# Kernel tuning notes

Hardware: AMD Instinct MI355X
Metric: run time of the kernel (lower is better)

The kernel has to match this reference:

```python
import jax, jax.numpy as jnp
import numpy as np

B, S, D = 8, 1024, 1024      # batch, seq, input_dim (= d_model)
H, E = 16, 64                # n_heads, d_embed (H*E == D)


def setup_inputs() -> dict:
    key = jax.random.key(0)
    ks = jax.random.split(key, 12)
    sd = 1.0 / np.sqrt(D)
    inp = {
        "X1": jax.random.normal(ks[0], (B, S, D), jnp.float32),
        "X2": jax.random.normal(ks[1], (B, S, D), jnp.float32),
        # Linear params stored as [in, out]
        "Wq": jax.random.uniform(ks[2], (D, H * E), jnp.float32, -sd, sd),
        "bq": jax.random.uniform(ks[3], (H * E,), jnp.float32, -sd, sd),
        "Wk": jax.random.uniform(ks[4], (D, H * E), jnp.float32, -sd, sd),
        "bk": jax.random.uniform(ks[5], (H * E,), jnp.float32, -sd, sd),
        "Wv": jax.random.uniform(ks[6], (D, H * E), jnp.float32, -sd, sd),
        "bv": jax.random.uniform(ks[7], (H * E,), jnp.float32, -sd, sd),
        "Wo": jax.random.uniform(ks[8], (H * E, D), jnp.float32, -sd, sd),
        "bo": jax.random.uniform(ks[9], (D,), jnp.float32, -sd, sd),
    }
    return inp


def reference(X1, X2, Wq, bq, Wk, bk, Wv, bv, Wo, bo):
    b, s, _ = X1.shape

    def split(x):  # [B,S,H*E] -> [B,H,S,E]
        return x.reshape(b, s, H, E).transpose(0, 2, 1, 3)

    Q = split(X1 @ Wq + bq)
    K = split(X2 @ Wk + bk)
    V = split(X2 @ Wv + bv)

    # Faithful quirk: d_k = K.shape[0] AFTER split_heads == batch size
    scores = jnp.einsum("bhqe,bhke->bhqk", Q, K) / jnp.sqrt(jnp.float32(b))

    # masked=True: tril then replace exact zeros with -1e9 (source quirk)
    tri = jnp.tril(jnp.ones((s, s), jnp.float32))
    scores = scores * tri
    scores = jnp.where(scores == 0.0, jnp.float32(-1e9), scores)

    # torch.nn.Softmax() with no dim on 4D input -> legacy dim=1 (heads axis)
    attn = jax.nn.softmax(scores, axis=1)

    out = jnp.einsum("bhqk,bhke->bhqe", attn, V)
    out = out.transpose(0, 2, 1, 3).reshape(b, s, H * E)  # combine heads
    return out @ Wo + bo
```

## Files before the change

kernel.cpp:

```cpp
#include <hip/hip_runtime.h>
#include <cstdint>


typedef unsigned short u16;
typedef unsigned int   u32;
typedef __attribute__((ext_vector_type(8))) __bf16         bf16x8;
typedef __attribute__((ext_vector_type(8))) unsigned short ushort8;
typedef __attribute__((ext_vector_type(4))) float          f32x4;

#define S_ 1024
#define D_ 1024
#define H_ 16
#define E_ 64

__device__ __forceinline__ float b2f(u16 h) {
  union { u32 u; float f; } v; v.u = ((u32)h) << 16; return v.f;
}
__device__ __forceinline__ u16 f2b(float f) {
  union { float f; u32 u; } v; v.f = f;
  u32 r = v.u + 0x7fffu + ((v.u >> 16) & 1u);
  return (u16)(r >> 16);
}

typedef const __attribute__((address_space(1))) u32 gu32;
typedef       __attribute__((address_space(3))) u32 lu32;

__device__ __forceinline__ void gload_lds16(const u16* g, u16* l) {
  __builtin_amdgcn_global_load_lds((gu32*)(uintptr_t)g, (lu32*)(uintptr_t)l,
                                   16, 0, 0);
}

__global__ __launch_bounds__(256, 1) void cvt_bf16(
    const float* __restrict__ src, u16* __restrict__ dst)
{
  const size_t i = (size_t)blockIdx.x * 256 + threadIdx.x;
  float4 a = ((const float4*)src)[2 * i];
  float4 b = ((const float4*)src)[2 * i + 1];
  ushort8 o;
  o[0] = f2b(a.x); o[1] = f2b(a.y); o[2] = f2b(a.z); o[3] = f2b(a.w);
  o[4] = f2b(b.x); o[5] = f2b(b.y); o[6] = f2b(b.z); o[7] = f2b(b.w);
  ((ushort8*)dst)[i] = o;
}

__global__ __launch_bounds__(256, 1) void trans_cvt_w(
    const float* __restrict__ W, u16* __restrict__ Wt)
{
  __shared__ u16 t[64][72];
  const int k0 = blockIdx.x * 64, n0 = blockIdx.y * 64;
  const int row = threadIdx.x >> 3;
  const int cs  = (threadIdx.x & 7) * 8;
#pragma unroll
  for (int p = 0; p < 2; ++p) {
    int r = row + p * 32;
    const float* Wp = W + (size_t)(k0 + r) * 1024 + n0 + cs;
    float4 a = *(const float4*)(Wp);
    float4 b = *(const float4*)(Wp + 4);
    u16* tp = &t[r][cs];
    tp[0] = f2b(a.x); tp[1] = f2b(a.y); tp[2] = f2b(a.z); tp[3] = f2b(a.w);
    tp[4] = f2b(b.x); tp[5] = f2b(b.y); tp[6] = f2b(b.z); tp[7] = f2b(b.w);
  }
  __syncthreads();
#pragma unroll
  for (int p = 0; p < 2; ++p) {
    int n = row + p * 32;
    ushort8 v;
#pragma unroll
    for (int i = 0; i < 8; ++i) v[i] = t[cs + i][n];
    *(ushort8*)(Wt + (size_t)(n0 + n) * 1024 + k0 + cs) = v;
  }
}

__global__ __launch_bounds__(256, 1) void gemm_bf16(
    const u16* __restrict__ A, const u16* __restrict__ Bt,
    const float* __restrict__ bias, void* __restrict__ Cv,
    int M, int N, int K, int out_f32)
{
  __shared__ u16 As[128 * 32];
  __shared__ u16 Bs[128 * 32];
  const int tid  = threadIdx.x;
  const int wave = tid >> 6;
  const int lane = tid & 63;
  const int quad = lane >> 4;
  const int l16  = lane & 15;
  const int m0   = (wave & 1) * 64;
  const int n0   = (wave >> 1) * 64;

  const u16* Ab = A  + (size_t)blockIdx.x * 128 * K;
  const u16* Bb = Bt + (size_t)blockIdx.y * 128 * K;

  f32x4 acc[4][4];
#pragma unroll
  for (int i = 0; i < 4; ++i)
#pragma unroll
    for (int j = 0; j < 4; ++j) acc[i][j] = (f32x4){0.f, 0.f, 0.f, 0.f};

  for (int kb = 0; kb < K; kb += 32) {
    __syncthreads();
#pragma unroll
    for (int p = 0; p < 2; ++p) {
      int seg = tid + p * 256;
      int row = seg >> 2, ks = seg & 3;
      gload_lds16(Ab + (size_t)row * K + kb + ks * 8, As + seg * 8);
      gload_lds16(Bb + (size_t)row * K + kb + ks * 8, Bs + seg * 8);
    }
    __builtin_amdgcn_s_waitcnt(0);
    __syncthreads();

    bf16x8 af[4], bfr[4];
#pragma unroll
    for (int i = 0; i < 4; ++i)
      af[i] = *(const bf16x8*)(As + (m0 + i * 16 + l16) * 32 + quad * 8);
#pragma unroll
    for (int j = 0; j < 4; ++j)
      bfr[j] = *(const bf16x8*)(Bs + (n0 + j * 16 + l16) * 32 + quad * 8);
#pragma unroll
    for (int i = 0; i < 4; ++i)
#pragma unroll
      for (int j = 0; j < 4; ++j)
        acc[i][j] = __builtin_amdgcn_mfma_f32_16x16x32_bf16(
            af[i], bfr[j], acc[i][j], 0, 0, 0);
  }

  float bv[4];
#pragma unroll
  for (int j = 0; j < 4; ++j)
    bv[j] = bias[(size_t)blockIdx.y * 128 + n0 + j * 16 + l16];

  if (out_f32) {
    float* C = (float*)Cv;
#pragma unroll
    for (int i = 0; i < 4; ++i) {
      int r = blockIdx.x * 128 + m0 + i * 16 + quad * 4;
#pragma unroll
      for (int j = 0; j < 4; ++j) {
        int c = blockIdx.y * 128 + n0 + j * 16 + l16;
#pragma unroll
        for (int reg = 0; reg < 4; ++reg)
          C[(size_t)(r + reg) * N + c] = acc[i][j][reg] + bv[j];
      }
    }
  } else {
    u16* C = (u16*)Cv;
#pragma unroll
    for (int i = 0; i < 4; ++i) {
      int r = blockIdx.x * 128 + m0 + i * 16 + quad * 4;
#pragma unroll
      for (int j = 0; j < 4; ++j) {
        int c = blockIdx.y * 128 + n0 + j * 16 + l16;
#pragma unroll
        for (int reg = 0; reg < 4; ++reg)
          C[(size_t)(r + reg) * N + c] = f2b(acc[i][j][reg] + bv[j]);
      }
    }
  }
}

__global__ __launch_bounds__(256, 1) void transpose_v(
    const u16* __restrict__ V, u16* __restrict__ Vt)
{
  __shared__ u16 t[64][72];
  const int s0 = blockIdx.x * 64;
  const int bh = blockIdx.y;
  const int b = bh >> 4, h = bh & 15;
  const int row = threadIdx.x >> 3;
  const int cs  = (threadIdx.x & 7) * 8;
#pragma unroll
  for (int p = 0; p < 2; ++p) {
    int s = row + p * 32;
    *(ushort8*)(&t[s][cs]) = *(const ushort8*)(
        V + ((size_t)(b * S_ + s0 + s)) * D_ + h * E_ + cs);
  }
  __syncthreads();
#pragma unroll
  for (int p = 0; p < 2; ++p) {
    int e = row + p * 32;
    ushort8 v;
#pragma unroll
    for (int i = 0; i < 8; ++i) v[i] = t[cs + i][e];
    *(ushort8*)(Vt + ((size_t)(bh * E_ + e)) * S_ + s0 + cs) = v;
  }
}

__global__ __launch_bounds__(1024, 4) void attn_headsoftmax(
    const u16* __restrict__ Qg,
    const u16* __restrict__ Kg,
    const u16* __restrict__ Vt,
    u16* __restrict__ AO)
{
  const int qt   = blockIdx.x;
  const int b    = blockIdx.y;
  const int tid  = threadIdx.x;
  const int h    = tid >> 6;
  const int lane = tid & 63;
  const int quad = lane >> 4;
  const int l16  = lane & 15;
  const int q0   = qt * 32;

  __shared__ float scf[16][32][33];
  __shared__ u16   at[16][32][40];

  bf16x8 qf[2][2];
  {
    const u16* Qb = Qg + ((size_t)(b * S_ + q0)) * D_ + h * E_;
#pragma unroll
    for (int i = 0; i < 2; ++i)
#pragma unroll
      for (int c = 0; c < 2; ++c)
        qf[i][c] = *(const bf16x8*)(Qb + (size_t)(i * 16 + l16) * D_ +
                                    c * 32 + quad * 8);
  }

  f32x4 oacc[2][4];
#pragma unroll
  for (int i = 0; i < 2; ++i)
#pragma unroll
    for (int nc = 0; nc < 4; ++nc) oacc[i][nc] = (f32x4){0.f, 0.f, 0.f, 0.f};

  const float inv_rsq8 = 0.35355339059327373f;

  for (int kt = 0; kt < 32; ++kt) {
    const int k0 = kt * 32;
    {
      const u16* Kb = Kg + ((size_t)(b * S_ + k0)) * D_ + h * E_;
      bf16x8 kf[2][2];
#pragma unroll
      for (int nc = 0; nc < 2; ++nc)
#pragma unroll
        for (int c = 0; c < 2; ++c)
          kf[nc][c] = *(const bf16x8*)(Kb + (size_t)(nc * 16 + l16) * D_ +
                                       c * 32 + quad * 8);
      f32x4 sacc[2][2];
#pragma unroll
      for (int i = 0; i < 2; ++i)
#pragma unroll
        for (int nc = 0; nc < 2; ++nc) sacc[i][nc] = (f32x4){0.f,0.f,0.f,0.f};
#pragma unroll
      for (int c = 0; c < 2; ++c)
#pragma unroll
        for (int i = 0; i < 2; ++i)
#pragma unroll
          for (int nc = 0; nc < 2; ++nc)
            sacc[i][nc] = __builtin_amdgcn_mfma_f32_16x16x32_bf16(
                qf[i][c], kf[nc][c], sacc[i][nc], 0, 0, 0);
#pragma unroll
      for (int i = 0; i < 2; ++i)
#pragma unroll
        for (int nc = 0; nc < 2; ++nc)
#pragma unroll
          for (int reg = 0; reg < 4; ++reg) {
            int qrow = i * 16 + quad * 4 + reg;
            int kcol = nc * 16 + l16;
            float s = sacc[i][nc][reg] * inv_rsq8;
            if ((k0 + kcol > q0 + qrow) || (s == 0.0f)) s = -1e9f;
            scf[h][qrow][kcol] = s;
          }
    }
    __syncthreads();
    {
      const int qq = tid >> 5, kk = tid & 31;
      float v[16];
      float m = -3.0e38f;
#pragma unroll
      for (int hh = 0; hh < 16; ++hh) {
        v[hh] = scf[hh][qq][kk];
        m = fmaxf(m, v[hh]);
      }
      float sum = 0.f;
#pragma unroll
      for (int hh = 0; hh < 16; ++hh) {
        v[hh] = __expf(v[hh] - m);
        sum += v[hh];
      }
      float inv = 1.0f / sum;
#pragma unroll
      for (int hh = 0; hh < 16; ++hh) at[hh][qq][kk] = f2b(v[hh] * inv);
    }
    __syncthreads();
    {
      bf16x8 af[2];
#pragma unroll
      for (int i = 0; i < 2; ++i)
        af[i] = *(const bf16x8*)(&at[h][i * 16 + l16][quad * 8]);
      const u16* Vb = Vt + ((size_t)((b * H_ + h) * E_)) * S_ + k0;
      bf16x8 vf[4];
#pragma unroll
      for (int nc = 0; nc < 4; ++nc)
        vf[nc] = *(const bf16x8*)(Vb + (size_t)(nc * 16 + l16) * S_ + quad * 8);
#pragma unroll
      for (int i = 0; i < 2; ++i)
#pragma unroll
        for (int nc = 0; nc < 4; ++nc)
          oacc[i][nc] = __builtin_amdgcn_mfma_f32_16x16x32_bf16(
              af[i], vf[nc], oacc[i][nc], 0, 0, 0);
    }
    __syncthreads();
  }

  u16* Ob = AO + ((size_t)(b * S_ + q0)) * D_ + h * E_;
#pragma unroll
  for (int i = 0; i < 2; ++i)
#pragma unroll
    for (int nc = 0; nc < 4; ++nc)
#pragma unroll
      for (int reg = 0; reg < 4; ++reg) {
        int qrow = i * 16 + quad * 4 + reg;
        int e    = nc * 16 + l16;
        Ob[(size_t)qrow * D_ + e] = f2b(oacc[i][nc][reg]);
      }
}

extern "C" void kernel_launch(void* const* d_in, const int* in_sizes, int n_in,
                              void* d_out, int out_size, void* d_ws,
                              size_t ws_size, hipStream_t stream)
{
  const float* X1 = (const float*)d_in[0];
  const float* X2 = (const float*)d_in[1];
  const float* Wq = (const float*)d_in[2];
  const float* bq = (const float*)d_in[3];
  const float* Wk = (const float*)d_in[4];
  const float* bk = (const float*)d_in[5];
  const float* Wv = (const float*)d_in[6];
  const float* bv = (const float*)d_in[7];
  const float* Wo = (const float*)d_in[8];
  const float* bo = (const float*)d_in[9];

  u16* X1b = (u16*)d_ws;
  u16* X2b = X1b + (8u << 20);
  u16* WtQ = X2b + (8u << 20);
  u16* WtK = WtQ + (1u << 20);
  u16* WtV = WtK + (1u << 20);
  u16* WtO = WtV + (1u << 20);
  u16* Qb  = WtO + (1u << 20);
  u16* Kb  = Qb + (8u << 20);
  u16* Vb  = Kb + (8u << 20);
  u16* Vtb = Vb + (8u << 20);
  u16* AOb = Vb;

  cvt_bf16<<<4096, 256, 0, stream>>>(X1, X1b);
  cvt_bf16<<<4096, 256, 0, stream>>>(X2, X2b);

  dim3 tg(16, 16);
  trans_cvt_w<<<tg, 256, 0, stream>>>(Wq, WtQ);
  trans_cvt_w<<<tg, 256, 0, stream>>>(Wk, WtK);
  trans_cvt_w<<<tg, 256, 0, stream>>>(Wv, WtV);
  trans_cvt_w<<<tg, 256, 0, stream>>>(Wo, WtO);

  dim3 gg(64, 8);
  gemm_bf16<<<gg, 256, 0, stream>>>(X1b, WtQ, bq, Qb, 8192, 1024, 1024, 0);
  gemm_bf16<<<gg, 256, 0, stream>>>(X2b, WtK, bk, Kb, 8192, 1024, 1024, 0);
  gemm_bf16<<<gg, 256, 0, stream>>>(X2b, WtV, bv, Vb, 8192, 1024, 1024, 0);

  transpose_v<<<dim3(16, 128), 256, 0, stream>>>(Vb, Vtb);

  attn_headsoftmax<<<dim3(32, 8), 1024, 0, stream>>>(Qb, Kb, Vtb, AOb);

  gemm_bf16<<<gg, 256, 0, stream>>>(AOb, WtO, bo, d_out, 8192, 1024, 1024, 1);
}
```

Measured before the change: 438.0 us.

## Skip fully-masked key tiles using uniform head-softmax and V suffix sums

Because masked scores are -1e9 in every head, the head-axis softmax is exactly 1/16 there, so key tiles entirely above the diagonal are replaced by a scaled column sum of V. The query tile shrinks to 16 rows with two heads per wave and 512-thread blocks, and the 1D grid pairs short and long causal tiles for load balance. This removes roughly half the score, softmax and PV work, at the cost of a serial strided reduction over the V suffix per lane.

```diff
diff --git a/kernel.cpp b/kernel.cpp
--- a/kernel.cpp
+++ b/kernel.cpp
@@ -181,47 +181,49 @@
   }
 }
 
-__global__ __launch_bounds__(1024, 4) void attn_headsoftmax(
+__global__ __launch_bounds__(512, 6) void attn_headsoftmax(
     const u16* __restrict__ Qg,
     const u16* __restrict__ Kg,
     const u16* __restrict__ Vt,
     u16* __restrict__ AO)
 {
-  const int qt   = blockIdx.x;
-  const int b    = blockIdx.y;
+  const int id   = blockIdx.x;
+  const int b    = id & 7;
+  const int x    = id >> 3;
+  const int qt   = (x < 32) ? x : 95 - x;
   const int tid  = threadIdx.x;
-  const int h    = tid >> 6;
+  const int h0   = (tid >> 6) * 2;
   const int lane = tid & 63;
   const int quad = lane >> 4;
   const int l16  = lane & 15;
-  const int q0   = qt * 32;
-
-  __shared__ float scf[16][32][33];
-  __shared__ u16   at[16][32][40];
+  const int q0   = qt * 16;
+
+  __shared__ float scf[16][16][33];
+  __shared__ u16   at[16][16][40];
 
   bf16x8 qf[2][2];
-  {
-    const u16* Qb = Qg + ((size_t)(b * S_ + q0)) * D_ + h * E_;
-#pragma unroll
-    for (int i = 0; i < 2; ++i)
-#pragma unroll
-      for (int c = 0; c < 2; ++c)
-        qf[i][c] = *(const bf16x8*)(Qb + (size_t)(i * 16 + l16) * D_ +
-                                    c * 32 + quad * 8);
+#pragma unroll
+  for (int hd = 0; hd < 2; ++hd) {
+    const u16* Qb = Qg + ((size_t)(b * S_ + q0)) * D_ + (h0 + hd) * E_;
+#pragma unroll
+    for (int c = 0; c < 2; ++c)
+      qf[hd][c] = *(const bf16x8*)(Qb + (size_t)l16 * D_ + c * 32 + quad * 8);
   }
 
   f32x4 oacc[2][4];
 #pragma unroll
-  for (int i = 0; i < 2; ++i)
-#pragma unroll
-    for (int nc = 0; nc < 4; ++nc) oacc[i][nc] = (f32x4){0.f, 0.f, 0.f, 0.f};
+  for (int hd = 0; hd < 2; ++hd)
+#pragma unroll
+    for (int nc = 0; nc < 4; ++nc) oacc[hd][nc] = (f32x4){0.f, 0.f, 0.f, 0.f};
 
   const float inv_rsq8 = 0.35355339059327373f;
 
-  for (int kt = 0; kt < 32; ++kt) {
+  const int ktEnd = (q0 + 15) >> 5;
+  for (int kt = 0; kt <= ktEnd; ++kt) {
     const int k0 = kt * 32;
-    {
-      const u16* Kb = Kg + ((size_t)(b * S_ + k0)) * D_ + h * E_;
+#pragma unroll
+    for (int hd = 0; hd < 2; ++hd) {
+      const u16* Kb = Kg + ((size_t)(b * S_ + k0)) * D_ + (h0 + hd) * E_;
       bf16x8 kf[2][2];
 #pragma unroll
       for (int nc = 0; nc < 2; ++nc)
@@ -229,31 +231,25 @@
         for (int c = 0; c < 2; ++c)
           kf[nc][c] = *(const bf16x8*)(Kb + (size_t)(nc * 16 + l16) * D_ +
                                        c * 32 + quad * 8);
-      f32x4 sacc[2][2];
-#pragma unroll
-      for (int i = 0; i < 2; ++i)
-#pragma unroll
-        for (int nc = 0; nc < 2; ++nc) sacc[i][nc] = (f32x4){0.f,0.f,0.f,0.f};
+      f32x4 sacc[2];
+      sacc[0] = (f32x4){0.f, 0.f, 0.f, 0.f};
+      sacc[1] = (f32x4){0.f, 0.f, 0.f, 0.f};
 #pragma unroll
       for (int c = 0; c < 2; ++c)
 #pragma unroll
-        for (int i = 0; i < 2; ++i)
-#pragma unroll
-          for (int nc = 0; nc < 2; ++nc)
-            sacc[i][nc] = __builtin_amdgcn_mfma_f32_16x16x32_bf16(
-                qf[i][c], kf[nc][c], sacc[i][nc], 0, 0, 0);
-#pragma unroll
-      for (int i = 0; i < 2; ++i)
-#pragma unroll
         for (int nc = 0; nc < 2; ++nc)
-#pragma unroll
-          for (int reg = 0; reg < 4; ++reg) {
-            int qrow = i * 16 + quad * 4 + reg;
-            int kcol = nc * 16 + l16;
-            float s = sacc[i][nc][reg] * inv_rsq8;
-            if ((k0 + kcol > q0 + qrow) || (s == 0.0f)) s = -1e9f;
-            scf[h][qrow][kcol] = s;
-          }
+          sacc[nc] = __builtin_amdgcn_mfma_f32_16x16x32_bf16(
+              qf[hd][c], kf[nc][c], sacc[nc], 0, 0, 0);
+#pragma unroll
+      for (int nc = 0; nc < 2; ++nc)
+#pragma unroll
+        for (int reg = 0; reg < 4; ++reg) {
+          int qrow = quad * 4 + reg;
+          int kcol = nc * 16 + l16;
+          float s = sacc[nc][reg] * inv_rsq8;
+          if ((k0 + kcol > q0 + qrow) || (s == 0.0f)) s = -1e9f;
+          scf[h0 + hd][qrow][kcol] = s;
+        }
     }
     __syncthreads();
     {
@@ -276,37 +272,67 @@
       for (int hh = 0; hh < 16; ++hh) at[hh][qq][kk] = f2b(v[hh] * inv);
     }
     __syncthreads();
-    {
-      bf16x8 af[2];
-#pragma unroll
-      for (int i = 0; i < 2; ++i)
-        af[i] = *(const bf16x8*)(&at[h][i * 16 + l16][quad * 8]);
-      const u16* Vb = Vt + ((size_t)((b * H_ + h) * E_)) * S_ + k0;
-      bf16x8 vf[4];
-#pragma unroll
-      for (int nc = 0; nc < 4; ++nc)
-        vf[nc] = *(const bf16x8*)(Vb + (size_t)(nc * 16 + l16) * S_ + quad * 8);
-#pragma unroll
-      for (int i = 0; i < 2; ++i)
-#pragma unroll
-        for (int nc = 0; nc < 4; ++nc)
-          oacc[i][nc] = __builtin_amdgcn_mfma_f32_16x16x32_bf16(
-              af[i], vf[nc], oacc[i][nc], 0, 0, 0);
-    }
-    __syncthreads();
-  }
-
-  u16* Ob = AO + ((size_t)(b * S_ + q0)) * D_ + h * E_;
-#pragma unroll
-  for (int i = 0; i < 2; ++i)
+#pragma unroll
+    for (int hd = 0; hd < 2; ++hd) {
+      bf16x8 af = *(const bf16x8*)(&at[h0 + hd][l16][quad * 8]);
+      const u16* Vb = Vt + ((size_t)((b * H_ + h0 + hd) * E_)) * S_ + k0;
+#pragma unroll
+      for (int nc = 0; nc < 4; ++nc) {
+        bf16x8 vf = *(const bf16x8*)(Vb + (size_t)(nc * 16 + l16) * S_ +
+                                     quad * 8);
+        oacc[hd][nc] = __builtin_amdgcn_mfma_f32_16x16x32_bf16(
+            af, vf, oacc[hd][nc], 0, 0, 0);
+      }
+    }
+    __syncthreads();
+  }
+
+  float suf[2][4];
+#pragma unroll
+  for (int hd = 0; hd < 2; ++hd)
+#pragma unroll
+    for (int nc = 0; nc < 4; ++nc) suf[hd][nc] = 0.f;
+  const int s0u = (ktEnd + 1) * 32;
+  if (s0u < S_) {
+    const int chunk = (S_ - s0u) >> 2;
+#pragma unroll
+    for (int hd = 0; hd < 2; ++hd)
+#pragma unroll
+      for (int nc = 0; nc < 4; ++nc) {
+        const u16* vp = Vt +
+            ((size_t)((b * H_ + h0 + hd) * E_ + nc * 16 + l16)) * S_ +
+            s0u + quad * chunk;
+        float a = 0.f;
+        for (int s = 0; s < chunk; s += 8) {
+          ushort8 v8 = *(const ushort8*)(vp + s);
+#pragma unroll
+          for (int j = 0; j < 8; ++j) a += b2f(v8[j]);
+        }
+        suf[hd][nc] = a;
+      }
+  }
+#pragma unroll
+  for (int hd = 0; hd < 2; ++hd)
+#pragma unroll
+    for (int nc = 0; nc < 4; ++nc) {
+      float a = suf[hd][nc];
+      a += __shfl_xor(a, 16);
+      a += __shfl_xor(a, 32);
+      suf[hd][nc] = a * 0.0625f;
+    }
+
+#pragma unroll
+  for (int hd = 0; hd < 2; ++hd) {
+    u16* Ob = AO + ((size_t)(b * S_ + q0)) * D_ + (h0 + hd) * E_;
 #pragma unroll
     for (int nc = 0; nc < 4; ++nc)
 #pragma unroll
       for (int reg = 0; reg < 4; ++reg) {
-        int qrow = i * 16 + quad * 4 + reg;
+        int qrow = quad * 4 + reg;
         int e    = nc * 16 + l16;
-        Ob[(size_t)qrow * D_ + e] = f2b(oacc[i][nc][reg]);
-      }
+        Ob[(size_t)qrow * D_ + e] = f2b(oacc[hd][nc][reg] + suf[hd][nc]);
+      }
+  }
 }
 
 extern "C" void kernel_launch(void* const* d_in, const int* in_sizes, int n_in,
@@ -352,7 +378,7 @@
 
   transpose_v<<<dim3(16, 128), 256, 0, stream>>>(Vb, Vtb);
 
-  attn_headsoftmax<<<dim3(32, 8), 1024, 0, stream>>>(Qb, Kb, Vtb, AOb);
+  attn_headsoftmax<<<dim3(512), 512, 0, stream>>>(Qb, Kb, Vtb, AOb);
 
   gemm_bf16<<<gg, 256, 0, stream>>>(AOb, WtO, bo, d_out, 8192, 1024, 1024, 1);
 }
```

After: 530.3 us. +21.1%, slower.

## Skip causal-masked key tiles via closed-form uniform head softmax and balance tiles

Applied to the files above, without the earlier changes.

Above the diagonal every head's score is -1e9, so the head-axis softmax there is exactly 1/16. The kernel now computes only key tiles up to the diagonal and adds the masked region as a scaled column sum of V. Each block takes two complementary query tiles, one for the even key tiles and one for the odd ones, to balance the triangular work, and prefetches V two steps ahead. Partial results are combined with fp32 atomics into a zeroed buffer, which adds a memset and a bf16 conversion pass.

```diff
diff --git a/kernel.cpp b/kernel.cpp
--- a/kernel.cpp
+++ b/kernel.cpp
@@ -185,128 +185,181 @@
     const u16* __restrict__ Qg,
     const u16* __restrict__ Kg,
     const u16* __restrict__ Vt,
-    u16* __restrict__ AO)
-{
-  const int qt   = blockIdx.x;
-  const int b    = blockIdx.y;
+    float* __restrict__ P)
+{
+  const int id   = blockIdx.x;
+  const int b    = id & 7;
+  const int j    = id >> 3;
   const int tid  = threadIdx.x;
   const int h    = tid >> 6;
   const int lane = tid & 63;
   const int quad = lane >> 4;
   const int l16  = lane & 15;
-  const int q0   = qt * 32;
-
-  __shared__ float scf[16][32][33];
+
+  __shared__ float scf[16][32][34];
   __shared__ u16   at[16][32][40];
 
-  bf16x8 qf[2][2];
-  {
-    const u16* Qb = Qg + ((size_t)(b * S_ + q0)) * D_ + h * E_;
+  const u16* Kh = Kg + (size_t)b * S_ * D_ + h * E_;
+  const u16* Vh = Vt + ((size_t)(b * H_ + h) * E_) * S_;
+
+  const float inv_rsq8 = 0.35355339059327373f;
+
+  auto run_task = [&](int qt, int parity, int do_tail) {
+    const int q0 = qt * 32;
+
+    bf16x8 qf[2][2];
+    {
+      const u16* Qb = Qg + ((size_t)(b * S_ + q0)) * D_ + h * E_;
+#pragma unroll
+      for (int i = 0; i < 2; ++i)
+#pragma unroll
+        for (int c = 0; c < 2; ++c)
+          qf[i][c] = *(const bf16x8*)(Qb + (size_t)(i * 16 + l16) * D_ +
+                                      c * 32 + quad * 8);
+    }
+
+    f32x4 oacc[2][4];
 #pragma unroll
     for (int i = 0; i < 2; ++i)
 #pragma unroll
-      for (int c = 0; c < 2; ++c)
-        qf[i][c] = *(const bf16x8*)(Qb + (size_t)(i * 16 + l16) * D_ +
-                                    c * 32 + quad * 8);
-  }
-
-  f32x4 oacc[2][4];
-#pragma unroll
-  for (int i = 0; i < 2; ++i)
-#pragma unroll
-    for (int nc = 0; nc < 4; ++nc) oacc[i][nc] = (f32x4){0.f, 0.f, 0.f, 0.f};
-
-  const float inv_rsq8 = 0.35355339059327373f;
-
-  for (int kt = 0; kt < 32; ++kt) {
-    const int k0 = kt * 32;
-    {
-      const u16* Kb = Kg + ((size_t)(b * S_ + k0)) * D_ + h * E_;
-      bf16x8 kf[2][2];
-#pragma unroll
-      for (int nc = 0; nc < 2; ++nc)
+      for (int nc = 0; nc < 4; ++nc) oacc[i][nc] = (f32x4){0.f,0.f,0.f,0.f};
+
+    bf16x8 vA[4], vB[4];
+    auto loadV = [&](int kt, bf16x8 (&vf)[4]) {
+      const u16* Vb = Vh + kt * 32;
+#pragma unroll
+      for (int nc = 0; nc < 4; ++nc)
+        vf[nc] = *(const bf16x8*)(Vb + (size_t)(nc * 16 + l16) * S_ +
+                                  quad * 8);
+    };
+
+    auto step = [&](int kt, bf16x8 (&vcur)[4], bf16x8 (&vnxt)[4]) {
+      const int k0 = kt * 32;
+      {
+        const u16* Kb = Kh + (size_t)k0 * D_;
+        bf16x8 kf[2][2];
+#pragma unroll
+        for (int nc = 0; nc < 2; ++nc)
+#pragma unroll
+          for (int c = 0; c < 2; ++c)
+            kf[nc][c] = *(const bf16x8*)(Kb + (size_t)(nc * 16 + l16) * D_ +
+                                         c * 32 + quad * 8);
+        f32x4 sacc[2][2];
+#pragma unroll
+        for (int i = 0; i < 2; ++i)
+#pragma unroll
+          for (int nc = 0; nc < 2; ++nc)
+            sacc[i][nc] = (f32x4){0.f, 0.f, 0.f, 0.f};
 #pragma unroll
         for (int c = 0; c < 2; ++c)
-          kf[nc][c] = *(const bf16x8*)(Kb + (size_t)(nc * 16 + l16) * D_ +
-                                       c * 32 + quad * 8);
-      f32x4 sacc[2][2];
-#pragma unroll
-      for (int i = 0; i < 2; ++i)
-#pragma unroll
-        for (int nc = 0; nc < 2; ++nc) sacc[i][nc] = (f32x4){0.f,0.f,0.f,0.f};
-#pragma unroll
-      for (int c = 0; c < 2; ++c)
+#pragma unroll
+          for (int i = 0; i < 2; ++i)
+#pragma unroll
+            for (int nc = 0; nc < 2; ++nc)
+              sacc[i][nc] = __builtin_amdgcn_mfma_f32_16x16x32_bf16(
+                  qf[i][c], kf[nc][c], sacc[i][nc], 0, 0, 0);
 #pragma unroll
         for (int i = 0; i < 2; ++i)
 #pragma unroll
           for (int nc = 0; nc < 2; ++nc)
-            sacc[i][nc] = __builtin_amdgcn_mfma_f32_16x16x32_bf16(
-                qf[i][c], kf[nc][c], sacc[i][nc], 0, 0, 0);
-#pragma unroll
-      for (int i = 0; i < 2; ++i)
-#pragma unroll
-        for (int nc = 0; nc < 2; ++nc)
-#pragma unroll
-          for (int reg = 0; reg < 4; ++reg) {
-            int qrow = i * 16 + quad * 4 + reg;
-            int kcol = nc * 16 + l16;
-            float s = sacc[i][nc][reg] * inv_rsq8;
-            if ((k0 + kcol > q0 + qrow) || (s == 0.0f)) s = -1e9f;
-            scf[h][qrow][kcol] = s;
+#pragma unroll
+            for (int reg = 0; reg < 4; ++reg) {
+              int qrow = i * 16 + quad * 4 + reg;
+              int kcol = nc * 16 + l16;
+              float s = sacc[i][nc][reg] * inv_rsq8;
+              if ((k0 + kcol > q0 + qrow) || (s == 0.0f)) s = -1e9f;
+              scf[h][qrow][kcol] = s;
+            }
+      }
+      if (kt + 2 <= qt) loadV(kt + 2, vnxt);
+      __syncthreads();
+      {
+        const int qq = tid >> 5, kk = tid & 31;
+        float v[16];
+        float m = -3.0e38f;
+#pragma unroll
+        for (int hh = 0; hh < 16; ++hh) {
+          v[hh] = scf[hh][qq][kk];
+          m = fmaxf(m, v[hh]);
+        }
+        float sum = 0.f;
+#pragma unroll
+        for (int hh = 0; hh < 16; ++hh) {
+          v[hh] = __expf(v[hh] - m);
+          sum += v[hh];
+        }
+        float inv = 1.0f / sum;
+#pragma unroll
+        for (int hh = 0; hh < 16; ++hh) at[hh][qq][kk] = f2b(v[hh] * inv);
+      }
+      __syncthreads();
+      {
+        bf16x8 af[2];
+#pragma unroll
+        for (int i = 0; i < 2; ++i)
+          af[i] = *(const bf16x8*)(&at[h][i * 16 + l16][quad * 8]);
+#pragma unroll
+        for (int i = 0; i < 2; ++i)
+#pragma unroll
+          for (int nc = 0; nc < 4; ++nc)
+            oacc[i][nc] = __builtin_amdgcn_mfma_f32_16x16x32_bf16(
+                af[i], vcur[nc], oacc[i][nc], 0, 0, 0);
+      }
+    };
+
+    int kt = parity;
+    if (kt <= qt) {
+      loadV(kt, vA);
+      while (true) {
+        step(kt, vA, vB); kt += 2; if (kt > qt) break;
+        step(kt, vB, vA); kt += 2; if (kt > qt) break;
+      }
+    }
+
+    float suf[4] = {0.f, 0.f, 0.f, 0.f};
+    if (do_tail) {
+      const int s0u = q0 + 32;
+      if (s0u < S_) {
+        const int chunk = (S_ - s0u) >> 2;
+#pragma unroll
+        for (int nc = 0; nc < 4; ++nc) {
+          const u16* vp = Vh + (size_t)(nc * 16 + l16) * S_ + s0u +
+                          quad * chunk;
+          float a = 0.f;
+          for (int s = 0; s < chunk; s += 8) {
+            ushort8 v8 = *(const ushort8*)(vp + s);
+#pragma unroll
+            for (int jj = 0; jj < 8; ++jj) a += b2f(v8[jj]);
           }
-    }
-    __syncthreads();
-    {
-      const int qq = tid >> 5, kk = tid & 31;
-      float v[16];
-      float m = -3.0e38f;
-#pragma unroll
-      for (int hh = 0; hh < 16; ++hh) {
-        v[hh] = scf[hh][qq][kk];
-        m = fmaxf(m, v[hh]);
-      }
-      float sum = 0.f;
-#pragma unroll
-      for (int hh = 0; hh < 16; ++hh) {
-        v[hh] = __expf(v[hh] - m);
-        sum += v[hh];
-      }
-      float inv = 1.0f / sum;
-#pragma unroll
-      for (int hh = 0; hh < 16; ++hh) at[hh][qq][kk] = f2b(v[hh] * inv);
-    }
-    __syncthreads();
-    {
-      bf16x8 af[2];
-#pragma unroll
-      for (int i = 0; i < 2; ++i)
-        af[i] = *(const bf16x8*)(&at[h][i * 16 + l16][quad * 8]);
-      const u16* Vb = Vt + ((size_t)((b * H_ + h) * E_)) * S_ + k0;
-      bf16x8 vf[4];
+          suf[nc] = a;
+        }
+#pragma unroll
+        for (int nc = 0; nc < 4; ++nc) {
+          float a = suf[nc];
+          a += __shfl_xor(a, 16);
+          a += __shfl_xor(a, 32);
+          suf[nc] = a * 0.0625f;
+        }
+      }
+    }
+
+    float* Pb = P + ((size_t)(b * S_ + q0)) * D_ + h * E_;
+#pragma unroll
+    for (int i = 0; i < 2; ++i)
 #pragma unroll
       for (int nc = 0; nc < 4; ++nc)
-        vf[nc] = *(const bf16x8*)(Vb + (size_t)(nc * 16 + l16) * S_ + quad * 8);
-#pragma unroll
-      for (int i = 0; i < 2; ++i)
-#pragma unroll
-        for (int nc = 0; nc < 4; ++nc)
-          oacc[i][nc] = __builtin_amdgcn_mfma_f32_16x16x32_bf16(
-              af[i], vf[nc], oacc[i][nc], 0, 0, 0);
-    }
-    __syncthreads();
-  }
-
-  u16* Ob = AO + ((size_t)(b * S_ + q0)) * D_ + h * E_;
-#pragma unroll
-  for (int i = 0; i < 2; ++i)
-#pragma unroll
-    for (int nc = 0; nc < 4; ++nc)
-#pragma unroll
-      for (int reg = 0; reg < 4; ++reg) {
-        int qrow = i * 16 + quad * 4 + reg;
-        int e    = nc * 16 + l16;
-        Ob[(size_t)qrow * D_ + e] = f2b(oacc[i][nc][reg]);
-      }
+#pragma unroll
+        for (int reg = 0; reg < 4; ++reg) {
+          int qrow = i * 16 + quad * 4 + reg;
+          int e    = nc * 16 + l16;
+          unsafeAtomicAdd(&Pb[(size_t)qrow * D_ + e],
+                          oacc[i][nc][reg] + suf[nc]);
+        }
+  };
+
+  run_task(j, 0, 0);
+  __syncthreads();
+  run_task(31 - j, 1, 1);
 }
 
 extern "C" void kernel_launch(void* const* d_in, const int* in_sizes, int n_in,
@@ -334,6 +387,7 @@
   u16* Kb  = Qb + (8u << 20);
   u16* Vb  = Kb + (8u << 20);
   u16* Vtb = Vb + (8u << 20);
+  float* P = (float*)d_ws;
   u16* AOb = Vb;
 
   cvt_bf16<<<4096, 256, 0, stream>>>(X1, X1b);
@@ -352,7 +406,11 @@
 
   transpose_v<<<dim3(16, 128), 256, 0, stream>>>(Vb, Vtb);
 
-  attn_headsoftmax<<<dim3(32, 8), 1024, 0, stream>>>(Qb, Kb, Vtb, AOb);
+  hipMemsetAsync(P, 0, (size_t)8192 * 1024 * 4, stream);
+
+  attn_headsoftmax<<<dim3(256), 1024, 0, stream>>>(Qb, Kb, Vtb, P);
+
+  cvt_bf16<<<4096, 256, 0, stream>>>(P, AOb);
 
   gemm_bf16<<<gg, 256, 0, stream>>>(AOb, WtO, bo, d_out, 8192, 1024, 1024, 1);
 }
```

Result: slower. 523.2 us (+19.5%).

## Process 64-key tiles per iteration with bf16 score staging and batch-interleaved grid

Applied to the files above, without the earlier changes.

The attention loop now handles 64 keys per iteration instead of 32, which halves the number of block-wide barriers per query tile. The score staging buffer is stored as bf16 instead of fp32 so the wider tile still fits in shared memory. The grid is flattened so consecutive blocks map to different batches. Storing scores in bf16 before the cross-head softmax loses precision, and the interleaved ordering changes L2 locality for K and V.

```diff
diff --git a/kernel.cpp b/kernel.cpp
--- a/kernel.cpp
+++ b/kernel.cpp
@@ -187,8 +187,9 @@
     const u16* __restrict__ Vt,
     u16* __restrict__ AO)
 {
-  const int qt   = blockIdx.x;
-  const int b    = blockIdx.y;
+  const int id   = blockIdx.x;
+  const int b    = id & 7;
+  const int qt   = id >> 3;
   const int tid  = threadIdx.x;
   const int h    = tid >> 6;
   const int lane = tid & 63;
@@ -196,8 +197,13 @@
   const int l16  = lane & 15;
   const int q0   = qt * 32;
 
-  __shared__ float scf[16][32][33];
-  __shared__ u16   at[16][32][40];
+  __shared__ u16 scf[16][32][66];
+  __shared__ u16 at[16][32][72];
+
+  const u16* Kh = Kg + (size_t)b * S_ * D_ + h * E_;
+  const u16* Vh = Vt + ((size_t)(b * H_ + h) * E_) * S_;
+
+  const float inv_rsq8 = 0.35355339059327373f;
 
   bf16x8 qf[2][2];
   {
@@ -216,12 +222,12 @@
 #pragma unroll
     for (int nc = 0; nc < 4; ++nc) oacc[i][nc] = (f32x4){0.f, 0.f, 0.f, 0.f};
 
-  const float inv_rsq8 = 0.35355339059327373f;
-
-  for (int kt = 0; kt < 32; ++kt) {
-    const int k0 = kt * 32;
-    {
-      const u16* Kb = Kg + ((size_t)(b * S_ + k0)) * D_ + h * E_;
+  for (int kt = 0; kt < 16; ++kt) {
+    const int k0 = kt * 64;
+#pragma unroll
+    for (int c2 = 0; c2 < 2; ++c2) {
+      const int ks0 = k0 + c2 * 32;
+      const u16* Kb = Kh + (size_t)ks0 * D_;
       bf16x8 kf[2][2];
 #pragma unroll
       for (int nc = 0; nc < 2; ++nc)
@@ -233,7 +239,8 @@
 #pragma unroll
       for (int i = 0; i < 2; ++i)
 #pragma unroll
-        for (int nc = 0; nc < 2; ++nc) sacc[i][nc] = (f32x4){0.f,0.f,0.f,0.f};
+        for (int nc = 0; nc < 2; ++nc)
+          sacc[i][nc] = (f32x4){0.f, 0.f, 0.f, 0.f};
 #pragma unroll
       for (int c = 0; c < 2; ++c)
 #pragma unroll
@@ -251,41 +258,47 @@
             int qrow = i * 16 + quad * 4 + reg;
             int kcol = nc * 16 + l16;
             float s = sacc[i][nc][reg] * inv_rsq8;
-            if ((k0 + kcol > q0 + qrow) || (s == 0.0f)) s = -1e9f;
-            scf[h][qrow][kcol] = s;
+            if ((ks0 + kcol > q0 + qrow) || (s == 0.0f)) s = -1e9f;
+            scf[h][qrow][c2 * 32 + kcol] = f2b(s);
           }
     }
     __syncthreads();
     {
       const int qq = tid >> 5, kk = tid & 31;
-      float v[16];
-      float m = -3.0e38f;
-#pragma unroll
-      for (int hh = 0; hh < 16; ++hh) {
-        v[hh] = scf[hh][qq][kk];
-        m = fmaxf(m, v[hh]);
+#pragma unroll
+      for (int c2 = 0; c2 < 2; ++c2) {
+        const int kk2 = c2 * 32 + kk;
+        float v[16];
+        float m = -3.0e38f;
+#pragma unroll
+        for (int hh = 0; hh < 16; ++hh) {
+          v[hh] = b2f(scf[hh][qq][kk2]);
+          m = fmaxf(m, v[hh]);
+        }
+        float sum = 0.f;
+#pragma unroll
+        for (int hh = 0; hh < 16; ++hh) {
+          v[hh] = __expf(v[hh] - m);
+          sum += v[hh];
+        }
+        float inv = 1.0f / sum;
+#pragma unroll
+        for (int hh = 0; hh < 16; ++hh) at[hh][qq][kk2] = f2b(v[hh] * inv);
       }
-      float sum = 0.f;
-#pragma unroll
-      for (int hh = 0; hh < 16; ++hh) {
-        v[hh] = __expf(v[hh] - m);
-        sum += v[hh];
-      }
-      float inv = 1.0f / sum;
-#pragma unroll
-      for (int hh = 0; hh < 16; ++hh) at[hh][qq][kk] = f2b(v[hh] * inv);
-    }
-    __syncthreads();
-    {
+    }
+    __syncthreads();
+#pragma unroll
+    for (int c2 = 0; c2 < 2; ++c2) {
       bf16x8 af[2];
 #pragma unroll
       for (int i = 0; i < 2; ++i)
-        af[i] = *(const bf16x8*)(&at[h][i * 16 + l16][quad * 8]);
-      const u16* Vb = Vt + ((size_t)((b * H_ + h) * E_)) * S_ + k0;
+        af[i] = *(const bf16x8*)(&at[h][i * 16 + l16][c2 * 32 + quad * 8]);
+      const u16* Vb = Vh + k0 + c2 * 32;
       bf16x8 vf[4];
 #pragma unroll
       for (int nc = 0; nc < 4; ++nc)
-        vf[nc] = *(const bf16x8*)(Vb + (size_t)(nc * 16 + l16) * S_ + quad * 8);
+        vf[nc] = *(const bf16x8*)(Vb + (size_t)(nc * 16 + l16) * S_ +
+                                  quad * 8);
 #pragma unroll
       for (int i = 0; i < 2; ++i)
 #pragma unroll
@@ -352,7 +365,7 @@
 
   transpose_v<<<dim3(16, 128), 256, 0, stream>>>(Vb, Vtb);
 
-  attn_headsoftmax<<<dim3(32, 8), 1024, 0, stream>>>(Qb, Kb, Vtb, AOb);
+  attn_headsoftmax<<<dim3(256), 1024, 0, stream>>>(Qb, Kb, Vtb, AOb);
 
   gemm_bf16<<<gg, 256, 0, stream>>>(AOb, WtO, bo, d_out, 8192, 1024, 1024, 1);
 }
```

Measured after the change: 440.6 us. About the same (+0.6%).
